# Kernel optimization log

Hardware: AMD Instinct MI355X
Metric: run time of the kernel (lower is better)

Reference implementation:

```python
import jax, jax.numpy as jnp
import numpy as np

N, E, D = 50000, 512000, 128

def mish(x):
    return x * jnp.tanh(jax.nn.softplus(x))

def ln(x, g, b):
    m = jnp.mean(x, axis=-1, keepdims=True)
    v = jnp.var(x, axis=-1, keepdims=True)
    return (x - m) / jnp.sqrt(v + 1e-5) * g + b

def setup_inputs():
    key = jax.random.key(0)
    ks = jax.random.split(key, 16)
    W = lambda k, i, o: jax.random.normal(k, (i, o), jnp.float32) * 0.02
    z = jnp.zeros((D,), jnp.float32)
    o = jnp.ones((D,), jnp.float32)
    return {
        "node_feat": jax.random.normal(ks[0], (N, D), jnp.float32),
        "coord_feat": jax.random.normal(ks[1], (N, D), jnp.float32),
        "Wq": W(ks[2], D, D), "bq": z, "gq": o, "beq": z,
        "Wk": W(ks[3], D, D), "bk": z, "gk": o, "bek": z,
        "Wm1": W(ks[4], D, D), "bm1": z, "gm": o, "bem": z,
        "Wm2": W(ks[5], D, D), "bm2": z,
        "Wb1": W(ks[6], D, D), "bb1": z, "gb": o, "beb": z,
        "Wb2": W(ks[7], D, D), "bb2": z,
        "Ww1": W(ks[8], D, D), "bw1": z, "gw": o, "bew": z,
        "Ww2": W(ks[9], D, D), "bw2": z,
        "Wn1": W(ks[10], 2 * D, D), "bn1": z,
        "Wn2": W(ks[11], D, D), "bn2": z,
        "Wc1": W(ks[12], D, D), "bc1": z,
        "Wc2": W(ks[13], D, D),
        "src": jax.random.randint(ks[14], (E,), 0, N, jnp.int32),
        "dst": jax.random.randint(ks[15], (E,), 0, N, jnp.int32),
    }

def reference(node_feat, coord_feat, Wq, bq, gq, beq, Wk, bk, gk, bek,
              Wm1, bm1, gm, bem, Wm2, bm2, Wb1, bb1, gb, beb, Wb2, bb2,
              Ww1, bw1, gw, bew, Ww2, bw2, Wn1, bn1, Wn2, bn2, Wc1, bc1, Wc2,
              src, dst):
    # linear_q / linear_k on coord features: Linear -> LayerNorm -> Mish
    q = mish(ln(coord_feat @ Wq + bq, gq, beq))   # [N, D]
    k = mish(ln(coord_feat @ Wk + bk, gk, bek))   # [N, D]
    # u_sub_v('q','k'): per-edge q[src] - k[dst]
    rel = q[src] - k[dst]                          # [E, D]
    radial = jnp.sum(rel * rel, axis=-1, keepdims=True)  # [E, 1]
    rel = rel / jnp.sqrt(radial + 1e-8)
    # relative position encodings from dst coord features
    xd = coord_feat[dst]                           # [E, D]
    pem = mish(ln(xd @ Wm1 + bm1, gm, bem)) @ Wm2 + bm2
    peb = mish(ln(xd @ Wb1 + bb1, gb, beb)) @ Wb2 + bb2
    rel = rel * pem + peb
    # weight_encoding MLP
    w = mish(ln(rel @ Ww1 + bw1, gw, bew)) @ Ww2 + bw2  # [E, D]
    # dgl.softmax_edges over a single graph: softmax across the edge axis
    w = jax.nn.softmax(w, axis=0)
    # update_all(copy_e, sum): scatter-add edge weights to destination nodes
    h_neigh = jax.ops.segment_sum(w, dst, num_segments=N)  # [N, D]
    h = mish(jnp.concatenate([node_feat, h_neigh], axis=-1) @ Wn1 + bn1) @ Wn2 + bn2
    x = mish(coord_feat @ Wc1 + bc1) @ Wc2
    return (h, x)
```

## Files before the change

### kernel.cpp

```cpp
#include <hip/hip_runtime.h>
#include <cstdint>
#include <cstddef>

#define DN 128
#define NND 50000
#define NED 512000

typedef __attribute__((ext_vector_type(8))) short bf8;
typedef __attribute__((ext_vector_type(4))) float f4;

__device__ __forceinline__ unsigned short f2bf(float f){
  union { float f; unsigned int u; } c; c.f = f;
  unsigned int r = c.u + 0x7fffu + ((c.u >> 16) & 1u);
  return (unsigned short)(r >> 16);
}
__device__ __forceinline__ float bf2f(unsigned short u){
  union { unsigned int u; float f; } c; c.u = ((unsigned int)u) << 16;
  return c.f;
}
__device__ __forceinline__ float mishf(float x){
  float e = __expf(x);
  float u = 1.f + e;
  float u2 = u * u;
  float t = (u2 - 1.f) / (u2 + 1.f);
  return x * ((x > 20.f) ? 1.f : t);
}

#define MFMA16(a, b, c) __builtin_amdgcn_mfma_f32_16x16x32_bf16((a), (b), (c), 0, 0, 0)

__device__ __forceinline__ bf8 lds_frag(const unsigned short* base, int row, int rowStrideB, int kElem){
  int byte = row * rowStrideB + kElem * 2;
  byte ^= (row & 7) << 4;
  return *(const bf8*)((const char*)base + byte);
}
__device__ __forceinline__ bf8 gfrag(const unsigned short* W, int n, int K, int kElem){
  return *(const bf8*)(W + (size_t)n * K + kElem);
}

template<int OUT_BF16>
__device__ __forceinline__ void store_tile(void* outp, int nrows, int r0,
                                           int wr, int wc, int g, int s,
                                           const f4 (&A)[2][4]){
#pragma unroll
  for (int rt = 0; rt < 2; ++rt)
#pragma unroll
    for (int ct = 0; ct < 4; ++ct)
#pragma unroll
      for (int reg = 0; reg < 4; ++reg){
        int row = r0 + wr*32 + rt*16 + g*4 + reg;
        if (row < nrows){
          int col = wc*64 + ct*16 + s;
          float v = A[rt][ct][reg];
          if constexpr (OUT_BF16 != 0)
            ((unsigned short*)outp)[(size_t)row*DN + col] = f2bf(v);
          else
            ((float*)outp)[(size_t)row*DN + col] = v;
        }
      }
}

template<int HAS_LN, int HAS_G2, int OUT_BF16>
__global__ __launch_bounds__(256, 2)
void node_chain(const float* __restrict__ X,
                const unsigned short* __restrict__ W1T,
                const float* __restrict__ b1,
                const float* __restrict__ gam,
                const float* __restrict__ bet,
                const unsigned short* __restrict__ W2T,
                const float* __restrict__ b2,
                void* __restrict__ outp, int nrows)
{
  __shared__ unsigned short Ash[64 * DN];
  __shared__ unsigned short Tsh[64 * DN];
  __shared__ float rowsum[64][2];
  __shared__ float rowsq[64][2];

  const int tid = threadIdx.x;
  const int r0 = blockIdx.x * 64;

  {
    int r = tid >> 2, c4 = tid & 3;
    int grow = r0 + r; if (grow >= nrows) grow = nrows - 1;
    const f4* sp = (const f4*)(X + (size_t)grow * DN + c4 * 32);
#pragma unroll
    for (int j = 0; j < 4; ++j){
      f4 v0 = sp[2*j], v1 = sp[2*j+1];
      bf8 o;
#pragma unroll
      for (int q = 0; q < 4; ++q){ o[q] = (short)f2bf(v0[q]); o[4+q] = (short)f2bf(v1[q]); }
      int byte = r*256 + c4*64 + j*16; byte ^= (r & 7) << 4;
      *(bf8*)((char*)Ash + byte) = o;
    }
  }
  __syncthreads();

  const int lane = tid & 63, w = tid >> 6;
  const int wr = w >> 1, wc = w & 1;
  const int g = lane >> 4, s = lane & 15;

  float b1v[4], gv[4], bev[4];
#pragma unroll
  for (int ct = 0; ct < 4; ++ct){
    int n = wc*64 + ct*16 + s;
    b1v[ct] = b1[n];
    if constexpr (HAS_LN != 0){ gv[ct] = gam[n]; bev[ct] = bet[n]; }
  }

  f4 acc[2][4];
#pragma unroll
  for (int rt = 0; rt < 2; ++rt)
#pragma unroll
    for (int ct = 0; ct < 4; ++ct){ f4 t = {b1v[ct], b1v[ct], b1v[ct], b1v[ct]}; acc[rt][ct] = t; }

  bf8 a[2][4];
#pragma unroll
  for (int rt = 0; rt < 2; ++rt)
#pragma unroll
    for (int kk = 0; kk < 4; ++kk)
      a[rt][kk] = lds_frag(Ash, wr*32 + rt*16 + s, 256, kk*32 + g*8);

#pragma unroll
  for (int ct = 0; ct < 4; ++ct){
    int n = wc*64 + ct*16 + s;
#pragma unroll
    for (int kk = 0; kk < 4; ++kk){
      bf8 b = gfrag(W1T, n, DN, kk*32 + g*8);
      acc[0][ct] = MFMA16(a[0][kk], b, acc[0][ct]);
      acc[1][ct] = MFMA16(a[1][kk], b, acc[1][ct]);
    }
  }

  if constexpr (HAS_LN != 0){
#pragma unroll
    for (int rt = 0; rt < 2; ++rt)
#pragma unroll
      for (int reg = 0; reg < 4; ++reg){
        float sm = acc[rt][0][reg] + acc[rt][1][reg] + acc[rt][2][reg] + acc[rt][3][reg];
        float sq = acc[rt][0][reg]*acc[rt][0][reg] + acc[rt][1][reg]*acc[rt][1][reg]
                 + acc[rt][2][reg]*acc[rt][2][reg] + acc[rt][3][reg]*acc[rt][3][reg];
#pragma unroll
        for (int m = 1; m < 16; m <<= 1){ sm += __shfl_xor(sm, m, 64); sq += __shfl_xor(sq, m, 64); }
        if (s == 0){
          int row = wr*32 + rt*16 + g*4 + reg;
          rowsum[row][wc] = sm; rowsq[row][wc] = sq;
        }
      }
    __syncthreads();
#pragma unroll
    for (int rt = 0; rt < 2; ++rt)
#pragma unroll
      for (int reg = 0; reg < 4; ++reg){
        int row = wr*32 + rt*16 + g*4 + reg;
        float sm = rowsum[row][0] + rowsum[row][1];
        float sq = rowsq[row][0] + rowsq[row][1];
        float mu = sm * (1.f/128.f);
        float var = sq * (1.f/128.f) - mu*mu;
        float rs = rsqrtf(var + 1e-5f);
#pragma unroll
        for (int ct = 0; ct < 4; ++ct)
          acc[rt][ct][reg] = (acc[rt][ct][reg] - mu) * rs * gv[ct] + bev[ct];
      }
  }

#pragma unroll
  for (int rt = 0; rt < 2; ++rt)
#pragma unroll
    for (int ct = 0; ct < 4; ++ct)
#pragma unroll
      for (int reg = 0; reg < 4; ++reg)
        acc[rt][ct][reg] = mishf(acc[rt][ct][reg]);

  if constexpr (HAS_G2 != 0){
#pragma unroll
    for (int rt = 0; rt < 2; ++rt)
#pragma unroll
      for (int ct = 0; ct < 4; ++ct)
#pragma unroll
        for (int reg = 0; reg < 4; ++reg){
          int row = wr*32 + rt*16 + g*4 + reg;
          int col = wc*64 + ct*16 + s;
          int byte = row*256 + col*2; byte ^= (row & 7) << 4;
          *(unsigned short*)((char*)Tsh + byte) = f2bf(acc[rt][ct][reg]);
        }
    __syncthreads();

    float b2v[4];
#pragma unroll
    for (int ct = 0; ct < 4; ++ct) b2v[ct] = b2 ? b2[wc*64 + ct*16 + s] : 0.f;
    f4 acc2[2][4];
#pragma unroll
    for (int rt = 0; rt < 2; ++rt)
#pragma unroll
      for (int ct = 0; ct < 4; ++ct){ f4 t = {b2v[ct], b2v[ct], b2v[ct], b2v[ct]}; acc2[rt][ct] = t; }
    bf8 a2[2][4];
#pragma unroll
    for (int rt = 0; rt < 2; ++rt)
#pragma unroll
      for (int kk = 0; kk < 4; ++kk)
        a2[rt][kk] = lds_frag(Tsh, wr*32 + rt*16 + s, 256, kk*32 + g*8);
#pragma unroll
    for (int ct = 0; ct < 4; ++ct){
      int n = wc*64 + ct*16 + s;
#pragma unroll
      for (int kk = 0; kk < 4; ++kk){
        bf8 b = gfrag(W2T, n, DN, kk*32 + g*8);
        acc2[0][ct] = MFMA16(a2[0][kk], b, acc2[0][ct]);
        acc2[1][ct] = MFMA16(a2[1][kk], b, acc2[1][ct]);
      }
    }
    store_tile<OUT_BF16>(outp, nrows, r0, wr, wc, g, s, acc2);
  } else {
    store_tile<OUT_BF16>(outp, nrows, r0, wr, wc, g, s, acc);
  }
}

__global__ __launch_bounds__(256, 2)
void edge_kernel(const unsigned short* __restrict__ qtab,
                 const unsigned short* __restrict__ ktab,
                 const unsigned short* __restrict__ mtab,
                 const unsigned short* __restrict__ btab,
                 const unsigned short* __restrict__ W1T,
                 const unsigned short* __restrict__ W2T,
                 const float* __restrict__ bw1,
                 const float* __restrict__ gwp,
                 const float* __restrict__ bewp,
                 const float* __restrict__ bw2,
                 const int* __restrict__ srcI,
                 const int* __restrict__ dstI,
                 float* __restrict__ hneigh,
                 float* __restrict__ colsum)
{
  __shared__ unsigned short Ash[64 * DN];
  __shared__ unsigned short Tsh[64 * DN];
  __shared__ float rowsum[64][2];
  __shared__ float rowsq[64][2];
  __shared__ int dsh[64];
  __shared__ float csh[DN];

  const int tid = threadIdx.x;
  const int e0 = blockIdx.x * 64;
  const int lane = tid & 63, w = tid >> 6;
  const int wr = w >> 1, wc = w & 1;
  const int g = lane >> 4, s = lane & 15;

  if (tid < 64) dsh[tid] = dstI[e0 + tid];
  if (tid < DN) csh[tid] = 0.f;

  bf8 B1[4][4], B2[4][4];
  float b1v[4], gv[4], bev[4], b2v[4];
#pragma unroll
  for (int ct = 0; ct < 4; ++ct){
    int n = wc*64 + ct*16 + s;
#pragma unroll
    for (int kk = 0; kk < 4; ++kk){
      B1[ct][kk] = gfrag(W1T, n, DN, kk*32 + g*8);
      B2[ct][kk] = gfrag(W2T, n, DN, kk*32 + g*8);
    }
    b1v[ct] = bw1[n]; gv[ct] = gwp[n]; bev[ct] = bewp[n]; b2v[ct] = bw2[n];
  }

  {
    int r = tid >> 2, c4 = tid & 3;
    int e = e0 + r;
    int sn = srcI[e], dn = dstI[e];
    const bf8* qp = (const bf8*)(qtab + (size_t)sn * DN + c4 * 32);
    const bf8* kp = (const bf8*)(ktab + (size_t)dn * DN + c4 * 32);
    const bf8* mp = (const bf8*)(mtab + (size_t)dn * DN + c4 * 32);
    const bf8* bp = (const bf8*)(btab + (size_t)dn * DN + c4 * 32);
    float rel[32]; float ss = 0.f;
#pragma unroll
    for (int j = 0; j < 4; ++j){
      bf8 qv = qp[j], kv = kp[j];
#pragma unroll
      for (int q = 0; q < 8; ++q){
        float d = bf2f((unsigned short)qv[q]) - bf2f((unsigned short)kv[q]);
        rel[j*8+q] = d; ss += d * d;
      }
    }
    ss += __shfl_xor(ss, 1, 64);
    ss += __shfl_xor(ss, 2, 64);
    float rinv = rsqrtf(ss + 1e-8f);
#pragma unroll
    for (int j = 0; j < 4; ++j){
      bf8 mv = mp[j], bv = bp[j];
      bf8 o;
#pragma unroll
      for (int q = 0; q < 8; ++q){
        float v = rel[j*8+q] * rinv * bf2f((unsigned short)mv[q]) + bf2f((unsigned short)bv[q]);
        o[q] = (short)f2bf(v);
      }
      int byte = r*256 + c4*64 + j*16; byte ^= (r & 7) << 4;
      *(bf8*)((char*)Ash + byte) = o;
    }
  }
  __syncthreads();

  f4 acc[2][4];
#pragma unroll
  for (int rt = 0; rt < 2; ++rt)
#pragma unroll
    for (int ct = 0; ct < 4; ++ct){ f4 t = {b1v[ct], b1v[ct], b1v[ct], b1v[ct]}; acc[rt][ct] = t; }
  bf8 a[2][4];
#pragma unroll
  for (int rt = 0; rt < 2; ++rt)
#pragma unroll
    for (int kk = 0; kk < 4; ++kk)
      a[rt][kk] = lds_frag(Ash, wr*32 + rt*16 + s, 256, kk*32 + g*8);
#pragma unroll
  for (int ct = 0; ct < 4; ++ct)
#pragma unroll
    for (int kk = 0; kk < 4; ++kk){
      acc[0][ct] = MFMA16(a[0][kk], B1[ct][kk], acc[0][ct]);
      acc[1][ct] = MFMA16(a[1][kk], B1[ct][kk], acc[1][ct]);
    }

#pragma unroll
  for (int rt = 0; rt < 2; ++rt)
#pragma unroll
    for (int reg = 0; reg < 4; ++reg){
      float sm = acc[rt][0][reg] + acc[rt][1][reg] + acc[rt][2][reg] + acc[rt][3][reg];
      float sq = acc[rt][0][reg]*acc[rt][0][reg] + acc[rt][1][reg]*acc[rt][1][reg]
               + acc[rt][2][reg]*acc[rt][2][reg] + acc[rt][3][reg]*acc[rt][3][reg];
#pragma unroll
      for (int m = 1; m < 16; m <<= 1){ sm += __shfl_xor(sm, m, 64); sq += __shfl_xor(sq, m, 64); }
      if (s == 0){
        int row = wr*32 + rt*16 + g*4 + reg;
        rowsum[row][wc] = sm; rowsq[row][wc] = sq;
      }
    }
  __syncthreads();
#pragma unroll
  for (int rt = 0; rt < 2; ++rt)
#pragma unroll
    for (int reg = 0; reg < 4; ++reg){
      int row = wr*32 + rt*16 + g*4 + reg;
      float sm = rowsum[row][0] + rowsum[row][1];
      float sq = rowsq[row][0] + rowsq[row][1];
      float mu = sm * (1.f/128.f);
      float var = sq * (1.f/128.f) - mu*mu;
      float rs = rsqrtf(var + 1e-5f);
#pragma unroll
      for (int ct = 0; ct < 4; ++ct)
        acc[rt][ct][reg] = mishf((acc[rt][ct][reg] - mu) * rs * gv[ct] + bev[ct]);
    }

#pragma unroll
  for (int rt = 0; rt < 2; ++rt)
#pragma unroll
    for (int ct = 0; ct < 4; ++ct)
#pragma unroll
      for (int reg = 0; reg < 4; ++reg){
        int row = wr*32 + rt*16 + g*4 + reg;
        int col = wc*64 + ct*16 + s;
        int byte = row*256 + col*2; byte ^= (row & 7) << 4;
        *(unsigned short*)((char*)Tsh + byte) = f2bf(acc[rt][ct][reg]);
      }
  __syncthreads();

  f4 p[2][4];
#pragma unroll
  for (int rt = 0; rt < 2; ++rt)
#pragma unroll
    for (int ct = 0; ct < 4; ++ct){ f4 t = {b2v[ct], b2v[ct], b2v[ct], b2v[ct]}; p[rt][ct] = t; }
  bf8 a2[2][4];
#pragma unroll
  for (int rt = 0; rt < 2; ++rt)
#pragma unroll
    for (int kk = 0; kk < 4; ++kk)
      a2[rt][kk] = lds_frag(Tsh, wr*32 + rt*16 + s, 256, kk*32 + g*8);
#pragma unroll
  for (int ct = 0; ct < 4; ++ct)
#pragma unroll
    for (int kk = 0; kk < 4; ++kk){
      p[0][ct] = MFMA16(a2[0][kk], B2[ct][kk], p[0][ct]);
      p[1][ct] = MFMA16(a2[1][kk], B2[ct][kk], p[1][ct]);
    }
#pragma unroll
  for (int rt = 0; rt < 2; ++rt)
#pragma unroll
    for (int ct = 0; ct < 4; ++ct)
#pragma unroll
      for (int reg = 0; reg < 4; ++reg)
        p[rt][ct][reg] = __expf(p[rt][ct][reg]);

#pragma unroll
  for (int ct = 0; ct < 4; ++ct){
    float cp = 0.f;
#pragma unroll
    for (int rt = 0; rt < 2; ++rt)
#pragma unroll
      for (int reg = 0; reg < 4; ++reg) cp += p[rt][ct][reg];
    cp += __shfl_xor(cp, 16, 64);
    cp += __shfl_xor(cp, 32, 64);
    if (g == 0) atomicAdd(&csh[wc*64 + ct*16 + s], cp);
  }

#pragma unroll
  for (int rt = 0; rt < 2; ++rt)
#pragma unroll
    for (int reg = 0; reg < 4; ++reg){
      int rl = wr*32 + rt*16 + g*4 + reg;
      float* hp = hneigh + (size_t)dsh[rl] * DN;
#pragma unroll
      for (int ct = 0; ct < 4; ++ct)
        atomicAdd(hp + (wc*64 + ct*16 + s), p[rt][ct][reg]);
    }
  __syncthreads();
  if (tid < DN) atomicAdd(&colsum[tid], csh[tid]);
}

__global__ __launch_bounds__(256, 2)
void final_h(const float* __restrict__ nodef,
             const float* __restrict__ hneigh,
             const float* __restrict__ colsum,
             const unsigned short* __restrict__ Wn1T,
             const float* __restrict__ bn1,
             const unsigned short* __restrict__ Wn2T,
             const float* __restrict__ bn2,
             float* __restrict__ outh)
{
  __shared__ unsigned short Ash[64 * 256];
  __shared__ unsigned short Tsh[64 * DN];

  const int tid = threadIdx.x;
  const int r0 = blockIdx.x * 64;
  {
    int r = tid >> 2, c4 = tid & 3;
    int grow = r0 + r; if (grow >= NND) grow = NND - 1;
    const f4* np = (const f4*)(nodef + (size_t)grow * DN + c4 * 32);
    const f4* hp = (const f4*)(hneigh + (size_t)grow * DN + c4 * 32);
    const f4* cp = (const f4*)(colsum + c4 * 32);
#pragma unroll
    for (int j = 0; j < 4; ++j){
      f4 v0 = np[2*j], v1 = np[2*j+1];
      bf8 o;
#pragma unroll
      for (int q = 0; q < 4; ++q){ o[q] = (short)f2bf(v0[q]); o[4+q] = (short)f2bf(v1[q]); }
      int byte = r*512 + c4*64 + j*16; byte ^= (r & 7) << 4;
      *(bf8*)((char*)Ash + byte) = o;
      f4 h0 = hp[2*j], h1 = hp[2*j+1];
      f4 c0 = cp[2*j], c1 = cp[2*j+1];
      bf8 o2;
#pragma unroll
      for (int q = 0; q < 4; ++q){
        o2[q]   = (short)f2bf(__fdividef(h0[q], c0[q]));
        o2[4+q] = (short)f2bf(__fdividef(h1[q], c1[q]));
      }
      int byte2 = r*512 + 256 + c4*64 + j*16; byte2 ^= (r & 7) << 4;
      *(bf8*)((char*)Ash + byte2) = o2;
    }
  }
  __syncthreads();

  const int lane = tid & 63, w = tid >> 6;
  const int wr = w >> 1, wc = w & 1;
  const int g = lane >> 4, s = lane & 15;

  float b1v[4], b2v[4];
#pragma unroll
  for (int ct = 0; ct < 4; ++ct){ int n = wc*64 + ct*16 + s; b1v[ct] = bn1[n]; b2v[ct] = bn2[n]; }

  f4 acc[2][4];
#pragma unroll
  for (int rt = 0; rt < 2; ++rt)
#pragma unroll
    for (int ct = 0; ct < 4; ++ct){ f4 t = {b1v[ct], b1v[ct], b1v[ct], b1v[ct]}; acc[rt][ct] = t; }

  bf8 a[2][8];
#pragma unroll
  for (int rt = 0; rt < 2; ++rt)
#pragma unroll
    for (int kk = 0; kk < 8; ++kk)
      a[rt][kk] = lds_frag(Ash, wr*32 + rt*16 + s, 512, kk*32 + g*8);
#pragma unroll
  for (int ct = 0; ct < 4; ++ct){
    int n = wc*64 + ct*16 + s;
#pragma unroll
    for (int kk = 0; kk < 8; ++kk){
      bf8 b = gfrag(Wn1T, n, 256, kk*32 + g*8);
      acc[0][ct] = MFMA16(a[0][kk], b, acc[0][ct]);
      acc[1][ct] = MFMA16(a[1][kk], b, acc[1][ct]);
    }
  }

#pragma unroll
  for (int rt = 0; rt < 2; ++rt)
#pragma unroll
    for (int ct = 0; ct < 4; ++ct)
#pragma unroll
      for (int reg = 0; reg < 4; ++reg){
        int row = wr*32 + rt*16 + g*4 + reg;
        int col = wc*64 + ct*16 + s;
        int byte = row*256 + col*2; byte ^= (row & 7) << 4;
        *(unsigned short*)((char*)Tsh + byte) = f2bf(mishf(acc[rt][ct][reg]));
      }
  __syncthreads();

  f4 acc2[2][4];
#pragma unroll
  for (int rt = 0; rt < 2; ++rt)
#pragma unroll
    for (int ct = 0; ct < 4; ++ct){ f4 t = {b2v[ct], b2v[ct], b2v[ct], b2v[ct]}; acc2[rt][ct] = t; }
  bf8 a2[2][4];
#pragma unroll
  for (int rt = 0; rt < 2; ++rt)
#pragma unroll
    for (int kk = 0; kk < 4; ++kk)
      a2[rt][kk] = lds_frag(Tsh, wr*32 + rt*16 + s, 256, kk*32 + g*8);
#pragma unroll
  for (int ct = 0; ct < 4; ++ct){
    int n = wc*64 + ct*16 + s;
#pragma unroll
    for (int kk = 0; kk < 4; ++kk){
      bf8 b = gfrag(Wn2T, n, DN, kk*32 + g*8);
      acc2[0][ct] = MFMA16(a2[0][kk], b, acc2[0][ct]);
      acc2[1][ct] = MFMA16(a2[1][kk], b, acc2[1][ct]);
    }
  }
  store_tile<0>((void*)outh, NND, r0, wr, wc, g, s, acc2);
}

struct WPrepArgs {
  const float* w[12];
  unsigned short* wt[12];
  int K[12];
};

__global__ void prep_weights(WPrepArgs a){
  int widx = blockIdx.y;
  int K = a.K[widx];
  int idx = blockIdx.x * 256 + threadIdx.x;
  if (idx >= DN * K) return;
  int kshift = (K == 256) ? 8 : 7;
  int n = idx >> kshift;
  int k = idx & (K - 1);
  a.wt[widx][idx] = f2bf(a.w[widx][(size_t)k * DN + n]);
}

extern "C" void kernel_launch(void* const* d_in, const int* in_sizes, int n_in,
                              void* d_out, int out_size, void* d_ws, size_t ws_size,
                              hipStream_t stream) {
  const float* node_feat = (const float*)d_in[0];
  const float* coordf    = (const float*)d_in[1];
  const float* Wq  = (const float*)d_in[2];
  const float* bq  = (const float*)d_in[3];
  const float* gq  = (const float*)d_in[4];
  const float* beq = (const float*)d_in[5];
  const float* Wk  = (const float*)d_in[6];
  const float* bk  = (const float*)d_in[7];
  const float* gk  = (const float*)d_in[8];
  const float* bek = (const float*)d_in[9];
  const float* Wm1 = (const float*)d_in[10];
  const float* bm1 = (const float*)d_in[11];
  const float* gm  = (const float*)d_in[12];
  const float* bem = (const float*)d_in[13];
  const float* Wm2 = (const float*)d_in[14];
  const float* bm2 = (const float*)d_in[15];
  const float* Wb1 = (const float*)d_in[16];
  const float* bb1 = (const float*)d_in[17];
  const float* gb  = (const float*)d_in[18];
  const float* beb = (const float*)d_in[19];
  const float* Wb2 = (const float*)d_in[20];
  const float* bb2 = (const float*)d_in[21];
  const float* Ww1 = (const float*)d_in[22];
  const float* bw1 = (const float*)d_in[23];
  const float* gw  = (const float*)d_in[24];
  const float* bew = (const float*)d_in[25];
  const float* Ww2 = (const float*)d_in[26];
  const float* bw2 = (const float*)d_in[27];
  const float* Wn1 = (const float*)d_in[28];
  const float* bn1 = (const float*)d_in[29];
  const float* Wn2 = (const float*)d_in[30];
  const float* bn2 = (const float*)d_in[31];
  const float* Wc1 = (const float*)d_in[32];
  const float* bc1 = (const float*)d_in[33];
  const float* Wc2 = (const float*)d_in[34];
  const int* srcI  = (const int*)d_in[35];
  const int* dstI  = (const int*)d_in[36];

  char* ws = (char*)d_ws;
  const size_t SZ_TAB = (size_t)NND * DN * 2;
  unsigned short* qt = (unsigned short*)(ws + 0 * SZ_TAB);
  unsigned short* kt = (unsigned short*)(ws + 1 * SZ_TAB);
  unsigned short* mt = (unsigned short*)(ws + 2 * SZ_TAB);
  unsigned short* bt = (unsigned short*)(ws + 3 * SZ_TAB);
  float* hneigh = (float*)(ws + 4 * SZ_TAB);
  float* colsum = (float*)(ws + 4 * SZ_TAB + (size_t)NND * DN * 4);
  unsigned short* wtb = (unsigned short*)(ws + 4 * SZ_TAB + (size_t)NND * DN * 4 + 1024);

  hipMemsetAsync(hneigh, 0, (size_t)NND * DN * 4 + 1024, stream);

  WPrepArgs pa;
  const float* wsrc[12] = {Wq, Wk, Wm1, Wm2, Wb1, Wb2, Ww1, Ww2, Wc1, Wc2, Wn2, Wn1};
  for (int i = 0; i < 12; ++i){
    pa.w[i] = wsrc[i];
    pa.wt[i] = wtb + (size_t)i * 16384;
    pa.K[i] = (i == 11) ? 256 : 128;
  }
  prep_weights<<<dim3(128, 12), 256, 0, stream>>>(pa);

  const int NB = (NND + 63) / 64;

  node_chain<1,0,1><<<NB, 256, 0, stream>>>(coordf, pa.wt[0], bq, gq, beq, nullptr, nullptr, (void*)qt, NND);
  node_chain<1,0,1><<<NB, 256, 0, stream>>>(coordf, pa.wt[1], bk, gk, bek, nullptr, nullptr, (void*)kt, NND);
  node_chain<1,1,1><<<NB, 256, 0, stream>>>(coordf, pa.wt[2], bm1, gm, bem, pa.wt[3], bm2, (void*)mt, NND);
  node_chain<1,1,1><<<NB, 256, 0, stream>>>(coordf, pa.wt[4], bb1, gb, beb, pa.wt[5], bb2, (void*)bt, NND);
  node_chain<0,1,0><<<NB, 256, 0, stream>>>(coordf, pa.wt[8], bc1, nullptr, nullptr, pa.wt[9], nullptr,
                                            (void*)((float*)d_out + (size_t)NND * DN), NND);

  edge_kernel<<<NED / 64, 256, 0, stream>>>(qt, kt, mt, bt, pa.wt[6], pa.wt[7],
                                            bw1, gw, bew, bw2, srcI, dstI, hneigh, colsum);

  final_h<<<NB, 256, 0, stream>>>(node_feat, hneigh, colsum, pa.wt[11], bn1, pa.wt[10], bn2, (float*)d_out);
}
```

Measured before the change: 609.2 us.

## Replace per-edge atomic scatter with CSR gather and interleave k/m/b tables

The edge kernel stops doing fp32 atomicAdds into a node-indexed buffer and instead writes each edge's exp weights as bf16 to a per-edge buffer. A CSR index over dst is built with count/scan/fill kernels, and a new gather kernel sums each node's incoming edges and applies the softmax column-sum normalisation before final_h. The k, m and b node tables are interleaved into one 384-wide row so a single dst lookup touches contiguous memory. This removes atomic contention and the large fp32 memset. In exchange it adds three CSR kernels, a single-block scan, an extra 131 MB bf16 write and read, and bf16 rounding of per-edge weights before summation.

```diff
diff --git a/kernel.cpp b/kernel.cpp
--- a/kernel.cpp
+++ b/kernel.cpp
@@ -39,7 +39,7 @@
 
 template<int OUT_BF16>
 __device__ __forceinline__ void store_tile(void* outp, int nrows, int r0,
-                                           int wr, int wc, int g, int s,
+                                           int wr, int wc, int g, int s, int ostride,
                                            const f4 (&A)[2][4]){
 #pragma unroll
   for (int rt = 0; rt < 2; ++rt)
@@ -52,9 +52,9 @@
           int col = wc*64 + ct*16 + s;
           float v = A[rt][ct][reg];
           if constexpr (OUT_BF16 != 0)
-            ((unsigned short*)outp)[(size_t)row*DN + col] = f2bf(v);
+            ((unsigned short*)outp)[(size_t)row*ostride + col] = f2bf(v);
           else
-            ((float*)outp)[(size_t)row*DN + col] = v;
+            ((float*)outp)[(size_t)row*ostride + col] = v;
         }
       }
 }
@@ -68,7 +68,7 @@
                 const float* __restrict__ bet,
                 const unsigned short* __restrict__ W2T,
                 const float* __restrict__ b2,
-                void* __restrict__ outp, int nrows)
+                void* __restrict__ outp, int ostride, int nrows)
 {
   __shared__ unsigned short Ash[64 * DN];
   __shared__ unsigned short Tsh[64 * DN];
@@ -208,17 +208,53 @@
         acc2[1][ct] = MFMA16(a2[1][kk], b, acc2[1][ct]);
       }
     }
-    store_tile<OUT_BF16>(outp, nrows, r0, wr, wc, g, s, acc2);
+    store_tile<OUT_BF16>(outp, nrows, r0, wr, wc, g, s, ostride, acc2);
   } else {
-    store_tile<OUT_BF16>(outp, nrows, r0, wr, wc, g, s, acc);
+    store_tile<OUT_BF16>(outp, nrows, r0, wr, wc, g, s, ostride, acc);
+  }
+}
+
+__global__ void csr_count(const int* __restrict__ dst, int* __restrict__ deg){
+  int e = blockIdx.x * 256 + threadIdx.x;
+  if (e < NED) atomicAdd(&deg[dst[e]], 1);
+}
+
+__global__ __launch_bounds__(1024) void csr_scan(const int* __restrict__ deg,
+                                                 int* __restrict__ ptr,
+                                                 int* __restrict__ fillctr){
+  __shared__ int ssum[1024];
+  const int t = threadIdx.x;
+  const int per = (NND + 1023) / 1024;
+  const int base = t * per;
+  int s = 0;
+  for (int i = 0; i < per; ++i){ int idx = base + i; if (idx < NND) s += deg[idx]; }
+  ssum[t] = s; __syncthreads();
+  for (int off = 1; off < 1024; off <<= 1){
+    int v = (t >= off) ? ssum[t - off] : 0;
+    __syncthreads();
+    ssum[t] += v;
+    __syncthreads();
+  }
+  int run = (t == 0) ? 0 : ssum[t - 1];
+  for (int i = 0; i < per; ++i){
+    int idx = base + i;
+    if (idx < NND){ ptr[idx] = run; fillctr[idx] = run; run += deg[idx]; }
+  }
+  if (t == 1023) ptr[NND] = run;
+}
+
+__global__ void csr_fill(const int* __restrict__ dst, int* __restrict__ fillctr,
+                         int* __restrict__ eidx){
+  int e = blockIdx.x * 256 + threadIdx.x;
+  if (e < NED){
+    int p = atomicAdd(&fillctr[dst[e]], 1);
+    eidx[p] = e;
   }
 }
 
 __global__ __launch_bounds__(256, 2)
 void edge_kernel(const unsigned short* __restrict__ qtab,
-                 const unsigned short* __restrict__ ktab,
-                 const unsigned short* __restrict__ mtab,
-                 const unsigned short* __restrict__ btab,
+                 const unsigned short* __restrict__ kmb,
                  const unsigned short* __restrict__ W1T,
                  const unsigned short* __restrict__ W2T,
                  const float* __restrict__ bw1,
@@ -227,14 +263,13 @@
                  const float* __restrict__ bw2,
                  const int* __restrict__ srcI,
                  const int* __restrict__ dstI,
-                 float* __restrict__ hneigh,
+                 unsigned short* __restrict__ pbuf,
                  float* __restrict__ colsum)
 {
   __shared__ unsigned short Ash[64 * DN];
   __shared__ unsigned short Tsh[64 * DN];
   __shared__ float rowsum[64][2];
   __shared__ float rowsq[64][2];
-  __shared__ int dsh[64];
   __shared__ float csh[DN];
 
   const int tid = threadIdx.x;
@@ -243,7 +278,6 @@
   const int wr = w >> 1, wc = w & 1;
   const int g = lane >> 4, s = lane & 15;
 
-  if (tid < 64) dsh[tid] = dstI[e0 + tid];
   if (tid < DN) csh[tid] = 0.f;
 
   bf8 B1[4][4], B2[4][4];
@@ -264,13 +298,12 @@
     int e = e0 + r;
     int sn = srcI[e], dn = dstI[e];
     const bf8* qp = (const bf8*)(qtab + (size_t)sn * DN + c4 * 32);
-    const bf8* kp = (const bf8*)(ktab + (size_t)dn * DN + c4 * 32);
-    const bf8* mp = (const bf8*)(mtab + (size_t)dn * DN + c4 * 32);
-    const bf8* bp = (const bf8*)(btab + (size_t)dn * DN + c4 * 32);
+    const unsigned short* kb = kmb + (size_t)dn * 384 + c4 * 32;
     float rel[32]; float ss = 0.f;
 #pragma unroll
     for (int j = 0; j < 4; ++j){
-      bf8 qv = qp[j], kv = kp[j];
+      bf8 qv = qp[j];
+      bf8 kv = *(const bf8*)(kb + j*8);
 #pragma unroll
       for (int q = 0; q < 8; ++q){
         float d = bf2f((unsigned short)qv[q]) - bf2f((unsigned short)kv[q]);
@@ -282,7 +315,8 @@
     float rinv = rsqrtf(ss + 1e-8f);
 #pragma unroll
     for (int j = 0; j < 4; ++j){
-      bf8 mv = mp[j], bv = bp[j];
+      bf8 mv = *(const bf8*)(kb + 128 + j*8);
+      bf8 bv = *(const bf8*)(kb + 256 + j*8);
       bf8 o;
 #pragma unroll
       for (int q = 0; q < 8; ++q){
@@ -395,24 +429,60 @@
     if (g == 0) atomicAdd(&csh[wc*64 + ct*16 + s], cp);
   }
 
-#pragma unroll
-  for (int rt = 0; rt < 2; ++rt)
-#pragma unroll
-    for (int reg = 0; reg < 4; ++reg){
-      int rl = wr*32 + rt*16 + g*4 + reg;
-      float* hp = hneigh + (size_t)dsh[rl] * DN;
-#pragma unroll
-      for (int ct = 0; ct < 4; ++ct)
-        atomicAdd(hp + (wc*64 + ct*16 + s), p[rt][ct][reg]);
-    }
-  __syncthreads();
+  __syncthreads();
+
+#pragma unroll
+  for (int rt = 0; rt < 2; ++rt)
+#pragma unroll
+    for (int ct = 0; ct < 4; ++ct)
+#pragma unroll
+      for (int reg = 0; reg < 4; ++reg){
+        int row = wr*32 + rt*16 + g*4 + reg;
+        int col = wc*64 + ct*16 + s;
+        int byte = row*256 + col*2; byte ^= (row & 7) << 4;
+        *(unsigned short*)((char*)Tsh + byte) = f2bf(p[rt][ct][reg]);
+      }
+  __syncthreads();
+
+  {
+    int r = tid >> 2, c4 = tid & 3;
+    unsigned short* dp = pbuf + (size_t)(e0 + r) * DN + c4 * 32;
+#pragma unroll
+    for (int j = 0; j < 4; ++j){
+      int byte = r*256 + c4*64 + j*16; byte ^= (r & 7) << 4;
+      bf8 v = *(const bf8*)((const char*)Tsh + byte);
+      *(bf8*)(dp + j*8) = v;
+    }
+  }
   if (tid < DN) atomicAdd(&colsum[tid], csh[tid]);
+}
+
+__global__ __launch_bounds__(256, 4)
+void gather_kernel(const unsigned short* __restrict__ pbuf,
+                   const int* __restrict__ ptr,
+                   const int* __restrict__ eidx,
+                   const float* __restrict__ colsum,
+                   unsigned short* __restrict__ hn)
+{
+  const int wv = threadIdx.x >> 6, lane = threadIdx.x & 63;
+  const int n = blockIdx.x * 4 + wv;
+  if (n >= NND) return;
+  const int beg = ptr[n], end = ptr[n + 1];
+  float a0 = 0.f, a1 = 0.f;
+  for (int i = beg; i < end; ++i){
+    int e = eidx[i];
+    unsigned int v = *(const unsigned int*)(pbuf + (size_t)e * DN + lane * 2);
+    a0 += bf2f((unsigned short)(v & 0xffffu));
+    a1 += bf2f((unsigned short)(v >> 16));
+  }
+  float c0 = colsum[lane*2], c1 = colsum[lane*2 + 1];
+  unsigned int o = ((unsigned int)f2bf(a1 / c1) << 16) | (unsigned int)f2bf(a0 / c0);
+  *(unsigned int*)(hn + (size_t)n * DN + lane * 2) = o;
 }
 
 __global__ __launch_bounds__(256, 2)
 void final_h(const float* __restrict__ nodef,
-             const float* __restrict__ hneigh,
-             const float* __restrict__ colsum,
+             const unsigned short* __restrict__ hn,
              const unsigned short* __restrict__ Wn1T,
              const float* __restrict__ bn1,
              const unsigned short* __restrict__ Wn2T,
@@ -428,8 +498,7 @@
     int r = tid >> 2, c4 = tid & 3;
     int grow = r0 + r; if (grow >= NND) grow = NND - 1;
     const f4* np = (const f4*)(nodef + (size_t)grow * DN + c4 * 32);
-    const f4* hp = (const f4*)(hneigh + (size_t)grow * DN + c4 * 32);
-    const f4* cp = (const f4*)(colsum + c4 * 32);
+    const bf8* hp = (const bf8*)(hn + (size_t)grow * DN + c4 * 32);
 #pragma unroll
     for (int j = 0; j < 4; ++j){
       f4 v0 = np[2*j], v1 = np[2*j+1];
@@ -438,14 +507,7 @@
       for (int q = 0; q < 4; ++q){ o[q] = (short)f2bf(v0[q]); o[4+q] = (short)f2bf(v1[q]); }
       int byte = r*512 + c4*64 + j*16; byte ^= (r & 7) << 4;
       *(bf8*)((char*)Ash + byte) = o;
-      f4 h0 = hp[2*j], h1 = hp[2*j+1];
-      f4 c0 = cp[2*j], c1 = cp[2*j+1];
-      bf8 o2;
-#pragma unroll
-      for (int q = 0; q < 4; ++q){
-        o2[q]   = (short)f2bf(__fdividef(h0[q], c0[q]));
-        o2[4+q] = (short)f2bf(__fdividef(h1[q], c1[q]));
-      }
+      bf8 o2 = hp[j];
       int byte2 = r*512 + 256 + c4*64 + j*16; byte2 ^= (r & 7) << 4;
       *(bf8*)((char*)Ash + byte2) = o2;
     }
@@ -517,7 +579,7 @@
       acc2[1][ct] = MFMA16(a2[1][kk], b, acc2[1][ct]);
     }
   }
-  store_tile<0>((void*)outh, NND, r0, wr, wc, g, s, acc2);
+  store_tile<0>((void*)outh, NND, r0, wr, wc, g, s, DN, acc2);
 }
 
 struct WPrepArgs {
@@ -579,16 +641,24 @@
   const int* dstI  = (const int*)d_in[36];
 
   char* ws = (char*)d_ws;
-  const size_t SZ_TAB = (size_t)NND * DN * 2;
-  unsigned short* qt = (unsigned short*)(ws + 0 * SZ_TAB);
-  unsigned short* kt = (unsigned short*)(ws + 1 * SZ_TAB);
-  unsigned short* mt = (unsigned short*)(ws + 2 * SZ_TAB);
-  unsigned short* bt = (unsigned short*)(ws + 3 * SZ_TAB);
-  float* hneigh = (float*)(ws + 4 * SZ_TAB);
-  float* colsum = (float*)(ws + 4 * SZ_TAB + (size_t)NND * DN * 4);
-  unsigned short* wtb = (unsigned short*)(ws + 4 * SZ_TAB + (size_t)NND * DN * 4 + 1024);
-
-  hipMemsetAsync(hneigh, 0, (size_t)NND * DN * 4 + 1024, stream);
+  size_t off = 0;
+  auto alloc = [&](size_t bytes) -> char* {
+    char* p = ws + off;
+    off += (bytes + 255) & ~(size_t)255;
+    return p;
+  };
+  unsigned short* qt     = (unsigned short*)alloc((size_t)NND * DN * 2);
+  unsigned short* kmb    = (unsigned short*)alloc((size_t)NND * 384 * 2);
+  unsigned short* pbuf   = (unsigned short*)alloc((size_t)NED * DN * 2);
+  float*          colsum = (float*)alloc(DN * 4);
+  int*            deg    = (int*)alloc((size_t)(NND + 1) * 4);
+  int*            ptr    = (int*)alloc((size_t)(NND + 1) * 4);
+  int*            fillctr= (int*)alloc((size_t)(NND + 1) * 4);
+  int*            eidx   = (int*)alloc((size_t)NED * 4);
+  unsigned short* wtb    = (unsigned short*)alloc((size_t)13 * 16384 * 2);
+
+  hipMemsetAsync(colsum, 0, DN * 4, stream);
+  hipMemsetAsync(deg, 0, (size_t)(NND + 1) * 4, stream);
 
   WPrepArgs pa;
   const float* wsrc[12] = {Wq, Wk, Wm1, Wm2, Wb1, Wb2, Ww1, Ww2, Wc1, Wc2, Wn2, Wn1};
@@ -599,17 +669,23 @@
   }
   prep_weights<<<dim3(128, 12), 256, 0, stream>>>(pa);
 
+  csr_count<<<(NED + 255) / 256, 256, 0, stream>>>(dstI, deg);
+  csr_scan<<<1, 1024, 0, stream>>>(deg, ptr, fillctr);
+  csr_fill<<<(NED + 255) / 256, 256, 0, stream>>>(dstI, fillctr, eidx);
+
   const int NB = (NND + 63) / 64;
 
-  node_chain<1,0,1><<<NB, 256, 0, stream>>>(coordf, pa.wt[0], bq, gq, beq, nullptr, nullptr, (void*)qt, NND);
-  node_chain<1,0,1><<<NB, 256, 0, stream>>>(coordf, pa.wt[1], bk, gk, bek, nullptr, nullptr, (void*)kt, NND);
-  node_chain<1,1,1><<<NB, 256, 0, stream>>>(coordf, pa.wt[2], bm1, gm, bem, pa.wt[3], bm2, (void*)mt, NND);
-  node_chain<1,1,1><<<NB, 256, 0, stream>>>(coordf, pa.wt[4], bb1, gb, beb, pa.wt[5], bb2, (void*)bt, NND);
+  node_chain<1,0,1><<<NB, 256, 0, stream>>>(coordf, pa.wt[0], bq, gq, beq, nullptr, nullptr, (void*)qt, DN, NND);
+  node_chain<1,0,1><<<NB, 256, 0, stream>>>(coordf, pa.wt[1], bk, gk, bek, nullptr, nullptr, (void*)kmb, 384, NND);
+  node_chain<1,1,1><<<NB, 256, 0, stream>>>(coordf, pa.wt[2], bm1, gm, bem, pa.wt[3], bm2, (void*)(kmb + 128), 384, NND);
+  node_chain<1,1,1><<<NB, 256, 0, stream>>>(coordf, pa.wt[4], bb1, gb, beb, pa.wt[5], bb2, (void*)(kmb + 256), 384, NND);
   node_chain<0,1,0><<<NB, 256, 0, stream>>>(coordf, pa.wt[8], bc1, nullptr, nullptr, pa.wt[9], nullptr,
-                                            (void*)((float*)d_out + (size_t)NND * DN), NND);
-
-  edge_kernel<<<NED / 64, 256, 0, stream>>>(qt, kt, mt, bt, pa.wt[6], pa.wt[7],
-                                            bw1, gw, bew, bw2, srcI, dstI, hneigh, colsum);
-
-  final_h<<<NB, 256, 0, stream>>>(node_feat, hneigh, colsum, pa.wt[11], bn1, pa.wt[10], bn2, (float*)d_out);
-}
+                                            (void*)((float*)d_out + (size_t)NND * DN), DN, NND);
+
+  edge_kernel<<<NED / 64, 256, 0, stream>>>(qt, kmb, pa.wt[6], pa.wt[7],
+                                            bw1, gw, bew, bw2, srcI, dstI, pbuf, colsum);
+
+  gather_kernel<<<(NND + 3) / 4, 256, 0, stream>>>(pbuf, ptr, eidx, colsum, qt);
+
+  final_h<<<NB, 256, 0, stream>>>(node_feat, qt, pa.wt[11], bn1, pa.wt[10], bn2, (float*)d_out);
+}
```

Result: slower. 652.3 us (+7.1%).
